# Kernel optimization log

Hardware: AMD Instinct MI355X
Metric: run time of the kernel (lower is better)

The kernel has to match this reference:

```python
import jax, jax.numpy as jnp
import numpy as np

V, E, H, D = 32000, 512, 512, 3          # vocab, embed_dim, hidden_dim, max_depth
PD = max(H // 4, 16)                      # policy depth-embed dim = 128
DEPTH_EMBED_SCALE = 0.01
SIB_SCALE = 1.0 / np.sqrt(H)              # sibling_scale default 1/sqrt(hidden_dim)
GREEDY_THRESHOLD = 0.5
PROB_MIN, PROB_MAX = 1e-7, 1.0 - 1e-7


def _ln(x, g, b, eps=1e-5):
    m = x.mean(-1, keepdims=True)
    v = jnp.var(x, axis=-1, keepdims=True)
    return (x - m) * jax.lax.rsqrt(v + eps) * g + b


def setup_inputs() -> dict:
    key = jax.random.key(0)
    ks = jax.random.split(key, 12)
    def n(k, shape, s=0.02):
        return jax.random.normal(k, shape, jnp.float32) * s
    return {
        "token_ids": jax.random.randint(ks[0], (4096,), 0, V),
        "emb": n(ks[1], (V, E)),                      # embedding table
        "proj_w": n(ks[2], (H, E), 0.04), "proj_b": jnp.zeros(H, jnp.float32),
        "cf_w": n(ks[3], (2 * H, H), 0.04), "cf_b": jnp.zeros(2 * H, jnp.float32),
        "in_g": jnp.ones(H, jnp.float32), "in_b": jnp.zeros(H, jnp.float32),   # policy input LayerNorm
        "pde": n(ks[4], (D + 1, PD), 0.01),           # policy depth embedding
        "f1w": n(ks[5], (H // 2, H + PD), 0.04), "f1b": jnp.zeros(H // 2, jnp.float32),
        "n1g": jnp.ones(H // 2, jnp.float32), "n1b": jnp.zeros(H // 2, jnp.float32),
        "f2w": n(ks[6], (H // 4, H // 2), 0.06), "f2b": jnp.zeros(H // 4, jnp.float32),
        "n2g": jnp.ones(H // 4, jnp.float32), "n2b": jnp.zeros(H // 4, jnp.float32),
        "pow_w": n(ks[7], (1, H // 4), 0.01), "pow_b": jnp.zeros(1, jnp.float32),
        "sib": n(ks[8], (2, H)),                      # sibling embeddings (left/right)
        "dep": n(ks[9], (D + 1, H), 0.01),            # tree depth embeddings
        "out_w": n(ks[10], (V, H), 0.04), "out_b": jnp.zeros(V, jnp.float32),
    }


def _forward(token_ids, emb, proj_w, proj_b, cf_w, cf_b, in_g, in_b, pde,
             f1w, f1b, n1g, n1b, f2w, f2b, n2g, n2b, pow_w, pow_b,
             sib, dep, out_w, out_b):
    # h0: project token embeddings to hidden space. [N, H]
    h0 = emb[token_ids] @ proj_w.T + proj_b
    nodes = h0[None]                      # level-0 nodes: [1, N, H]
    agg_sum = h0                          # running sum over all tree nodes
    agg_cnt = jnp.float32(1.0)
    alive = jnp.float32(1.0)              # cumulative greedy-expand mask
    for level in range(D):
        # growth policy on the level-mean hidden (+ scaled depth embedding)
        lh = nodes.mean(0) + DEPTH_EMBED_SCALE * dep[level]          # [N, H]
        hn = _ln(lh, in_g, in_b)
        de = jnp.broadcast_to(pde[min(level, D)], (hn.shape[0], PD))
        x = jnp.concatenate([hn, de], axis=-1)
        x = jax.nn.relu(_ln(x @ f1w.T + f1b, n1g, n1b))
        x = jax.nn.relu(_ln(x @ f2w.T + f2b, n2g, n2b))
        p = jax.nn.sigmoid((x @ pow_w.T + pow_b)[..., 0])             # [N]
        p_mean = jnp.clip(p, PROB_MIN, PROB_MAX).mean()
        alive = alive * (p_mean >= GREEDY_THRESHOLD).astype(jnp.float32)
        # binary child expansion: child_fc then chunk into left/right + sibling embeds
        cf = jnp.einsum('mnh,kh->mnk', nodes, cf_w) + cf_b            # [M, N, 2H]
        left = cf[..., :H] + SIB_SCALE * sib[0]
        right = cf[..., H:] + SIB_SCALE * sib[1]
        nodes = jnp.concatenate([left, right], axis=0)                # [2M, N, H]
        agg_sum = agg_sum + alive * nodes.sum(0)
        agg_cnt = agg_cnt + alive * jnp.float32(nodes.shape[0])
    pooled = agg_sum / jnp.maximum(agg_cnt, 1e-8)                     # mean pooling
    return pooled @ out_w.T + out_b                                   # [N, V]


def reference(token_ids, emb, proj_w, proj_b, cf_w, cf_b, in_g, in_b, pde,
              f1w, f1b, n1g, n1b, f2w, f2b, n2g, n2b, pow_w, pow_b,
              sib, dep, out_w, out_b):
    return _forward(token_ids, emb, proj_w, proj_b, cf_w, cf_b, in_g, in_b, pde,
                    f1w, f1b, n1g, n1b, f2w, f2b, n2g, n2b, pow_w, pow_b,
                    sib, dep, out_w, out_b)
```

## Files before the change

### kernel.cpp

```cpp
#include <hip/hip_runtime.h>

typedef unsigned short u16;
using bf16x8 = __attribute__((ext_vector_type(8))) short;
using f32x4  = __attribute__((ext_vector_type(4))) float;

#define SIB_SCALE_F 0.04419417382415922f

__device__ __forceinline__ u16 f2b(float f) {
  unsigned u = __builtin_bit_cast(unsigned, f);
  return (u16)((u + 0x7FFFu + ((u >> 16) & 1u)) >> 16);
}

__device__ __forceinline__ float wred(float v) {
  #pragma unroll
  for (int m = 1; m < 64; m <<= 1) v += __shfl_xor(v, m);
  return v;
}

__device__ __forceinline__ void gload16(const void* g, void* l) {
  __builtin_amdgcn_global_load_lds(
      (const __attribute__((address_space(1))) unsigned int*)g,
      (__attribute__((address_space(3))) unsigned int*)l, 16, 0, 0);
}

__global__ __launch_bounds__(256, 2) void gemmT(
    const u16* __restrict__ A, const u16* __restrict__ B,
    const float* __restrict__ bias,
    float* __restrict__ C, int M, int N, int K, int MT)
{
  __shared__ u16 lds[32768];
  const int t = threadIdx.x, w = t >> 6, lane = t & 63;
  const int wm = w >> 1, wn = w & 1;
  const int r16 = lane & 15, ks = lane >> 4;
  const int bn = blockIdx.y * 128;
  const int mg = blockIdx.x;
  const int stag = blockIdx.y & (MT - 1);

  auto stageT = [&](const u16* __restrict__ G, int grow0, int ktile, int buf, int base) {
    const int k0 = ktile << 6;
    u16* dst = lds + base + (buf << 13);
    #pragma unroll
    for (int j = 0; j < 4; ++j) {
      const int r = j * 32 + w * 8 + (lane >> 3);
      const int s = (lane & 7) ^ (r & 7);
      gload16(G + (size_t)(grow0 + r) * K + k0 + s * 8,
              dst + j * 2048 + w * 512);
    }
  };

  float4 biasv[4];
  #pragma unroll
  for (int n = 0; n < 4; ++n)
    biasv[n] = *(const float4*)(bias + bn + wn * 64 + n * 16 + ks * 4);

  f32x4 acc[4][4], pacc[4][4];
  #pragma unroll
  for (int m = 0; m < 4; ++m)
    #pragma unroll
    for (int n = 0; n < 4; ++n) {
      f32x4 z = {0.f, 0.f, 0.f, 0.f};
      acc[m][n] = z; pacc[m][n] = z;
    }
  int bmPrev = 0;

  {
    const int bm0 = (mg * MT + (stag & (MT - 1))) * 128;
    stageT(A, bm0, 0, 0, 0);
    stageT(B, bn, 0, 0, 16384);
    stageT(B, bn, 1, 1, 16384);
    asm volatile("s_waitcnt vmcnt(4)" ::: "memory");
    __builtin_amdgcn_sched_barrier(0);
    __builtin_amdgcn_s_barrier();
  }

  for (int mt = 0; mt < MT; ++mt) {
    const int bm = (mg * MT + ((mt + stag) & (MT - 1))) * 128;
    const int bmNext = (mg * MT + ((mt + 1 + stag) & (MT - 1))) * 128;

    #pragma unroll
    for (int kt = 0; kt < 8; ++kt) {
      const u16* Ab = lds + ((kt & 1) << 13);
      const u16* Bb = lds + 16384 + ((kt & 1) << 13);
      bf16x8 bfr[4][2];

      #pragma unroll
      for (int p = 0; p < 4; ++p) {
        bf16x8 af[2];
        {
          const int row = wm * 64 + p * 16 + r16;
          af[0] = *(const bf16x8*)(Ab + row * 64 + ((ks ^ (row & 7)) << 3));
          af[1] = *(const bf16x8*)(Ab + row * 64 + (((4 + ks) ^ (row & 7)) << 3));
        }
        if (p == 0) {
          #pragma unroll
          for (int n = 0; n < 4; ++n) {
            const int row = wn * 64 + n * 16 + r16;
            bfr[n][0] = *(const bf16x8*)(Bb + row * 64 + ((ks ^ (row & 7)) << 3));
            bfr[n][1] = *(const bf16x8*)(Bb + row * 64 + (((4 + ks) ^ (row & 7)) << 3));
          }
          if (kt < 7)             stageT(A, bm,     kt + 1, (kt + 1) & 1, 0);
          else if (mt < MT - 1)   stageT(A, bmNext, 0,      0,            0);
        }
        if (p == 1 && kt == 0 && mt > 0) {
          #pragma unroll
          for (int m = 0; m < 4; ++m) {
            const int grow = bmPrev + wm * 64 + m * 16 + r16;
            float* Crow = C + (size_t)grow * N;
            #pragma unroll
            for (int n = 0; n < 4; ++n) {
              const int gcol = bn + wn * 64 + n * 16 + ks * 4;
              f32x4 o;
              o[0] = pacc[m][n][0] + biasv[n].x;
              o[1] = pacc[m][n][1] + biasv[n].y;
              o[2] = pacc[m][n][2] + biasv[n].z;
              o[3] = pacc[m][n][3] + biasv[n].w;
              __builtin_nontemporal_store(o, (f32x4*)(Crow + gcol));
            }
          }
        }
        if (p == 2) {
          if (kt < 6)             stageT(B, bn, kt + 2,       kt & 1, 16384);
          else if (mt < MT - 1)   stageT(B, bn, (kt + 2) & 7, kt & 1, 16384);
        }
        if (p == 3) {
          if (kt == 0) {
            if (mt > 0) { asm volatile("s_waitcnt vmcnt(20)" ::: "memory"); }
            else        { asm volatile("s_waitcnt vmcnt(4)"  ::: "memory"); }
          } else if (kt < 6) {
            asm volatile("s_waitcnt vmcnt(4)" ::: "memory");
          } else if (kt == 6) {
            if (mt < MT - 1) { asm volatile("s_waitcnt vmcnt(4)" ::: "memory"); }
            else             { asm volatile("s_waitcnt vmcnt(0)" ::: "memory"); }
          } else {
            if (mt < MT - 1) { asm volatile("s_waitcnt vmcnt(4)" ::: "memory"); }
          }
          __builtin_amdgcn_sched_barrier(0);
        }
        __builtin_amdgcn_s_barrier();
        asm volatile("s_waitcnt lgkmcnt(0)" ::: "memory");
        __builtin_amdgcn_sched_barrier(0);
        __builtin_amdgcn_s_setprio(1);
        #pragma unroll
        for (int n = 0; n < 4; ++n) {
          acc[p][n] = __builtin_amdgcn_mfma_f32_16x16x32_bf16(bfr[n][0], af[0], acc[p][n], 0, 0, 0);
          acc[p][n] = __builtin_amdgcn_mfma_f32_16x16x32_bf16(bfr[n][1], af[1], acc[p][n], 0, 0, 0);
        }
        __builtin_amdgcn_s_setprio(0);
        __builtin_amdgcn_s_barrier();
      }
    }

    bmPrev = bm;
    #pragma unroll
    for (int m = 0; m < 4; ++m)
      #pragma unroll
      for (int n = 0; n < 4; ++n) {
        pacc[m][n] = acc[m][n];
        f32x4 z = {0.f, 0.f, 0.f, 0.f};
        acc[m][n] = z;
      }
  }

  #pragma unroll
  for (int m = 0; m < 4; ++m) {
    const int grow = bmPrev + wm * 64 + m * 16 + r16;
    float* Crow = C + (size_t)grow * N;
    #pragma unroll
    for (int n = 0; n < 4; ++n) {
      const int gcol = bn + wn * 64 + n * 16 + ks * 4;
      f32x4 o;
      o[0] = pacc[m][n][0] + biasv[n].x;
      o[1] = pacc[m][n][1] + biasv[n].y;
      o[2] = pacc[m][n][2] + biasv[n].z;
      o[3] = pacc[m][n][3] + biasv[n].w;
      __builtin_nontemporal_store(o, (f32x4*)(Crow + gcol));
    }
  }
}

template <bool GATHER>
__global__ __launch_bounds__(256) void gemm64(
    const float* __restrict__ Afp, const int* __restrict__ tok,
    const u16* __restrict__ A, const u16* __restrict__ B,
    const float* __restrict__ bias, int blvl, float bscale,
    float* __restrict__ C, u16* __restrict__ Cb,
    int M, int N, int K)
{
  __shared__ u16 ldsA[64 * 32];
  __shared__ u16 ldsB[128 * 32];
  const int t = threadIdx.x, w = t >> 6, lane = t & 63;
  const int r16 = lane & 15, ks = lane >> 4;

  const int nb = gridDim.x * gridDim.y;
  const int lid = blockIdx.y * gridDim.x + blockIdx.x;
  const int chunk = nb >> 3;
  const int nlid = (lid & 7) * chunk + (lid >> 3);
  const int bm = (nlid % gridDim.x) * 64;
  const int bn = (nlid / gridDim.x) * 128;

  const int srow = t >> 2, sslot = t & 3;

  f32x4 acc[4][2];
  #pragma unroll
  for (int m = 0; m < 4; ++m)
    #pragma unroll
    for (int n = 0; n < 2; ++n) {
      f32x4 z = {0.f, 0.f, 0.f, 0.f};
      acc[m][n] = z;
    }

  for (int k0 = 0; k0 < K; k0 += 32) {
    if (k0) __syncthreads();
    {
      const int row = srow;
      const int sl = sslot ^ ((row >> 1) & 3);
      if constexpr (GATHER) {
        const float* src = Afp + (size_t)tok[bm + row] * 512 + k0 + sl * 8;
        const float4 a0 = *(const float4*)src;
        const float4 a1 = *(const float4*)(src + 4);
        bf16x8 v;
        v[0] = (short)f2b(a0.x); v[1] = (short)f2b(a0.y);
        v[2] = (short)f2b(a0.z); v[3] = (short)f2b(a0.w);
        v[4] = (short)f2b(a1.x); v[5] = (short)f2b(a1.y);
        v[6] = (short)f2b(a1.z); v[7] = (short)f2b(a1.w);
        *(bf16x8*)(ldsA + t * 8) = v;
      } else {
        gload16(A + (size_t)(bm + row) * K + k0 + sl * 8, ldsA + w * 512);
      }
    }
    #pragma unroll
    for (int i = 0; i < 2; ++i) {
      const int row = i * 64 + srow;
      const int sl = sslot ^ ((row >> 1) & 3);
      gload16(B + (size_t)(bn + row) * K + k0 + sl * 8,
              ldsB + i * 2048 + w * 512);
    }
    __syncthreads();

    bf16x8 af[4], bfr[2];
    #pragma unroll
    for (int m = 0; m < 4; ++m) {
      const int row = m * 16 + r16;
      af[m] = *(const bf16x8*)(ldsA + row * 32 + ((ks ^ ((row >> 1) & 3)) << 3));
    }
    #pragma unroll
    for (int n = 0; n < 2; ++n) {
      const int row = w * 32 + n * 16 + r16;
      bfr[n] = *(const bf16x8*)(ldsB + row * 32 + ((ks ^ ((row >> 1) & 3)) << 3));
    }
    #pragma unroll
    for (int m = 0; m < 4; ++m)
      #pragma unroll
      for (int n = 0; n < 2; ++n)
        acc[m][n] = __builtin_amdgcn_mfma_f32_16x16x32_bf16(bfr[n], af[m], acc[m][n], 0, 0, 0);
  }

  const float* be = bias + (size_t)(bm >> 12) * blvl;
  #pragma unroll
  for (int m = 0; m < 4; ++m) {
    const int grow = bm + m * 16 + r16;
    #pragma unroll
    for (int n = 0; n < 2; ++n) {
      const int gcol = bn + w * 32 + n * 16 + ks * 4;
      const float4 bv = *(const float4*)(be + gcol);
      float4 o;
      o.x = acc[m][n][0] + bv.x * bscale;
      o.y = acc[m][n][1] + bv.y * bscale;
      o.z = acc[m][n][2] + bv.z * bscale;
      o.w = acc[m][n][3] + bv.w * bscale;
      const size_t idx = (size_t)grow * N + gcol;
      *(float4*)(C + idx) = o;
      if (Cb) {
        ushort4 ob = { f2b(o.x), f2b(o.y), f2b(o.z), f2b(o.w) };
        *(ushort4*)(Cb + idx) = ob;
      }
    }
  }
}

__global__ __launch_bounds__(256) void gemm_pool(
    const u16* __restrict__ A, const u16* __restrict__ B,
    const float* __restrict__ bias, float bscale,
    const float* __restrict__ h0f, const float* __restrict__ S1f,
    const float* __restrict__ S2f, const float* __restrict__ psum,
    u16* __restrict__ P,
    int M, int N, int K)
{
  __shared__ u16 ldsA[128 * 32];
  __shared__ u16 ldsB[128 * 32];
  const int t = threadIdx.x;
  const int w = t >> 6;
  const int lane = t & 63;
  const int wr = w >> 1, wc = w & 1;

  const int nb = gridDim.x * gridDim.y;
  const int lid = blockIdx.y * gridDim.x + blockIdx.x;
  const int chunk = nb >> 3;
  const int nlid = (lid & 7) * chunk + (lid >> 3);
  const int bx = nlid % gridDim.x, by = nlid / gridDim.x;

  const int bm = bx * 128, bn = by * 128;
  const int r16 = lane & 15, ks = lane >> 4;
  const int srow = t >> 2, sslot = t & 3;

  f32x4 acc[4][4];
  #pragma unroll
  for (int m = 0; m < 4; ++m)
    #pragma unroll
    for (int n = 0; n < 4; ++n) {
      f32x4 z = {0.f, 0.f, 0.f, 0.f};
      acc[m][n] = z;
    }

  for (int k0 = 0; k0 < K; k0 += 32) {
    if (k0) __syncthreads();
    #pragma unroll
    for (int i = 0; i < 2; ++i) {
      const int row = srow + i * 64;
      const int sl = sslot ^ ((row >> 1) & 3);
      gload16(A + (size_t)(bm + row) * K + k0 + sl * 8,
              ldsA + (i * 2048 + w * 512));
      gload16(B + (size_t)(bn + row) * K + k0 + sl * 8,
              ldsB + (i * 2048 + w * 512));
    }
    __syncthreads();

    bf16x8 af[4], bfr[4];
    #pragma unroll
    for (int m = 0; m < 4; ++m) {
      const int row = wr * 64 + m * 16 + r16;
      af[m] = *(const bf16x8*)(ldsA + row * 32 + ((ks ^ ((row >> 1) & 3)) << 3));
    }
    #pragma unroll
    for (int n = 0; n < 4; ++n) {
      const int row = wc * 64 + n * 16 + r16;
      bfr[n] = *(const bf16x8*)(ldsB + row * 32 + ((ks ^ ((row >> 1) & 3)) << 3));
    }
    #pragma unroll
    for (int m = 0; m < 4; ++m)
      #pragma unroll
      for (int n = 0; n < 4; ++n)
        acc[m][n] = __builtin_amdgcn_mfma_f32_16x16x32_bf16(bfr[n], af[m], acc[m][n], 0, 0, 0);
  }

  const float a0 = (psum[0] * (1.f / 4096.f) >= 0.5f) ? 1.f : 0.f;
  const float a1 = a0 * ((psum[1] * (1.f / 4096.f) >= 0.5f) ? 1.f : 0.f);
  const float a2 = a1 * ((psum[2] * (1.f / 4096.f) >= 0.5f) ? 1.f : 0.f);
  const float cnt = 1.f + a0 * 2.f + a1 * 4.f + a2 * 8.f;
  const float inv = 1.f / fmaxf(cnt, 1e-8f);

  #pragma unroll
  for (int m = 0; m < 4; ++m) {
    const int grow = bm + wr * 64 + m * 16 + r16;
    #pragma unroll
    for (int n = 0; n < 4; ++n) {
      const int gcol = bn + wc * 64 + n * 16 + ks * 4;
      const float4 bv = *(const float4*)(bias + gcol);
      float4 o;
      o.x = acc[m][n][0] + bv.x * bscale;
      o.y = acc[m][n][1] + bv.y * bscale;
      o.z = acc[m][n][2] + bv.z * bscale;
      o.w = acc[m][n][3] + bv.w * bscale;
      const size_t idx = (size_t)grow * N + gcol;
      const float4 h = *(const float4*)(h0f + idx);
      const float4 s1 = *(const float4*)(S1f + idx);
      const float4 s2 = *(const float4*)(S2f + idx);
      ushort4 ob;
      ob.x = f2b((h.x + a0 * s1.x + a1 * s2.x + a2 * o.x) * inv);
      ob.y = f2b((h.y + a0 * s1.y + a1 * s2.y + a2 * o.y) * inv);
      ob.z = f2b((h.z + a0 * s1.z + a1 * s2.z + a2 * o.z) * inv);
      ob.w = f2b((h.w + a0 * s1.w + a1 * s2.w + a2 * o.w) * inv);
      *(ushort4*)(P + idx) = ob;
    }
  }
}

__global__ __launch_bounds__(256) void prep_misc(
    const float* __restrict__ cf_w, const float* __restrict__ cf_b,
    const float* __restrict__ sib, const float* __restrict__ proj_w,
    const float* __restrict__ f1w, const float* __restrict__ f1b,
    const float* __restrict__ f2w, const float* __restrict__ pde,
    const float* __restrict__ out_w,
    u16* __restrict__ wsum_b, u16* __restrict__ projw_b,
    u16* __restrict__ f1w512b, u16* __restrict__ f2wb,
    float* __restrict__ cvec, float* __restrict__ psum,
    float* __restrict__ y1bias, u16* __restrict__ outw_b)
{
  const int b = blockIdx.x, t = threadIdx.x;
  if (b >= 676) {
    const int idx = (b - 676) * 256 + t;
    const float4 v = ((const float4*)out_w)[idx];
    ushort4 o = { f2b(v.x), f2b(v.y), f2b(v.z), f2b(v.w) };
    ((ushort4*)outw_b)[idx] = o;
  } else if (b < 256) {
    const int idx = b * 256 + t;
    const float4 a = ((const float4*)cf_w)[idx];
    const float4 c = ((const float4*)(cf_w + 262144))[idx];
    ushort4 o = { f2b(a.x + c.x), f2b(a.y + c.y), f2b(a.z + c.z), f2b(a.w + c.w) };
    ((ushort4*)wsum_b)[idx] = o;
  } else if (b < 512) {
    const int idx = (b - 256) * 256 + t;
    const float4 v = ((const float4*)proj_w)[idx];
    ushort4 o = { f2b(v.x), f2b(v.y), f2b(v.z), f2b(v.w) };
    ((ushort4*)projw_b)[idx] = o;
  } else if (b < 640) {
    const int fi = (b - 512) * 256 + t;
    const int row = fi >> 7, c4 = fi & 127;
    const float4 v = *(const float4*)(f1w + (size_t)row * 640 + c4 * 4);
    ushort4 o = { f2b(v.x), f2b(v.y), f2b(v.z), f2b(v.w) };
    ((ushort4*)f1w512b)[row * 128 + c4] = o;
  } else if (b < 672) {
    const int idx = (b - 640) * 256 + t;
    const float4 v = ((const float4*)f2w)[idx];
    ushort4 o = { f2b(v.x), f2b(v.y), f2b(v.z), f2b(v.w) };
    ((ushort4*)f2wb)[idx] = o;
  } else if (b < 675) {
    const int l = b - 672, j = t;
    const float* wrow = f1w + (size_t)j * 640 + 512;
    const float* p = pde + l * 128;
    float s = f1b[j];
    #pragma unroll 4
    for (int k = 0; k < 128; ++k) s += wrow[k] * p[k];
    y1bias[l * 256 + j] = s;
  } else {
    cvec[t]       = cf_b[t]       + cf_b[512 + t] + SIB_SCALE_F * (sib[t]       + sib[512 + t]);
    cvec[256 + t] = cf_b[256 + t] + cf_b[768 + t] + SIB_SCALE_F * (sib[256 + t] + sib[768 + t]);
    if (t < 3) psum[t] = 0.f;
  }
}

__global__ __launch_bounds__(256) void mean_ln_concat_b(
    const float* __restrict__ S0, const float* __restrict__ S1,
    const float* __restrict__ S2,
    const float* __restrict__ dep,
    const float* __restrict__ g, const float* __restrict__ b,
    u16* __restrict__ X)
{
  const int wid = threadIdx.x >> 6, lane = threadIdx.x & 63;
  const int gr = blockIdx.x * 4 + wid;
  const int l = gr >> 12, n = gr & 4095;
  const float* Sr = (l == 0 ? S0 : l == 1 ? S1 : S2) + (size_t)n * 512;
  const float invM = (l == 0 ? 1.f : l == 1 ? 0.5f : 0.25f);
  const float* depl = dep + 512 * l;
  const int c0 = lane * 8;
  float x[8];
  float s = 0.f, sq = 0.f;
  #pragma unroll
  for (int i = 0; i < 8; ++i) {
    const float v = Sr[c0 + i] * invM + 0.01f * depl[c0 + i];
    x[i] = v; s += v; sq += v * v;
  }
  s = wred(s); sq = wred(sq);
  const float mean = s * (1.f / 512.f);
  const float var = sq * (1.f / 512.f) - mean * mean;
  const float rs = rsqrtf(var + 1e-5f);
  ushort4 o0, o1;
  o0.x = f2b((x[0] - mean) * rs * g[c0 + 0] + b[c0 + 0]);
  o0.y = f2b((x[1] - mean) * rs * g[c0 + 1] + b[c0 + 1]);
  o0.z = f2b((x[2] - mean) * rs * g[c0 + 2] + b[c0 + 2]);
  o0.w = f2b((x[3] - mean) * rs * g[c0 + 3] + b[c0 + 3]);
  o1.x = f2b((x[4] - mean) * rs * g[c0 + 4] + b[c0 + 4]);
  o1.y = f2b((x[5] - mean) * rs * g[c0 + 5] + b[c0 + 5]);
  o1.z = f2b((x[6] - mean) * rs * g[c0 + 6] + b[c0 + 6]);
  o1.w = f2b((x[7] - mean) * rs * g[c0 + 7] + b[c0 + 7]);
  ushort4* Xr = (ushort4*)(X + (size_t)gr * 512);
  Xr[lane * 2]     = o0;
  Xr[lane * 2 + 1] = o1;
}

__global__ __launch_bounds__(256) void ln_relu_b256(
    const float* __restrict__ X, const float* __restrict__ g,
    const float* __restrict__ b, u16* __restrict__ O)
{
  const int wid = threadIdx.x >> 6, lane = threadIdx.x & 63;
  const int n = blockIdx.x * 4 + wid;
  const float* Xr = X + (size_t)n * 256;
  float x[4];
  float s = 0.f, sq = 0.f;
  #pragma unroll
  for (int i = 0; i < 4; ++i) {
    x[i] = Xr[lane * 4 + i]; s += x[i]; sq += x[i] * x[i];
  }
  s = wred(s); sq = wred(sq);
  const float mean = s * (1.f / 256.f);
  const float var = sq * (1.f / 256.f) - mean * mean;
  const float rs = rsqrtf(var + 1e-5f);
  ushort4 o;
  o.x = f2b(fmaxf((x[0] - mean) * rs * g[lane * 4 + 0] + b[lane * 4 + 0], 0.f));
  o.y = f2b(fmaxf((x[1] - mean) * rs * g[lane * 4 + 1] + b[lane * 4 + 1], 0.f));
  o.z = f2b(fmaxf((x[2] - mean) * rs * g[lane * 4 + 2] + b[lane * 4 + 2], 0.f));
  o.w = f2b(fmaxf((x[3] - mean) * rs * g[lane * 4 + 3] + b[lane * 4 + 3], 0.f));
  ((ushort4*)(O + (size_t)n * 256))[lane] = o;
}

__global__ __launch_bounds__(256) void ln_policy128(
    const float* __restrict__ Y2, const float* __restrict__ g,
    const float* __restrict__ b, const float* __restrict__ pw,
    const float* __restrict__ pb, float* __restrict__ psum)
{
  __shared__ float part[4];
  const int wid = threadIdx.x >> 6, lane = threadIdx.x & 63;
  const int gr = blockIdx.x * 4 + wid;
  const float* Xr = Y2 + (size_t)gr * 128;
  float x[2];
  float s = 0.f, sq = 0.f;
  #pragma unroll
  for (int i = 0; i < 2; ++i) {
    x[i] = Xr[lane * 2 + i]; s += x[i]; sq += x[i] * x[i];
  }
  s = wred(s); sq = wred(sq);
  const float mean = s * (1.f / 128.f);
  const float var = sq * (1.f / 128.f) - mean * mean;
  const float rs = rsqrtf(var + 1e-5f);
  float z = 0.f;
  #pragma unroll
  for (int i = 0; i < 2; ++i) {
    const int c = lane * 2 + i;
    const float v = fmaxf((x[i] - mean) * rs * g[c] + b[c], 0.f);
    z += v * pw[c];
  }
  z = wred(z);
  if (lane == 0) {
    const float p = 1.f / (1.f + expf(-(z + pb[0])));
    part[wid] = fminf(fmaxf(p, 1e-7f), 1.f - 1e-7f);
  }
  __syncthreads();
  if (threadIdx.x == 0)
    atomicAdd(psum + (gr >> 12), part[0] + part[1] + part[2] + part[3]);
}

extern "C" void kernel_launch(void* const* d_in, const int* in_sizes, int n_in,
                              void* d_out, int out_size, void* d_ws, size_t ws_size,
                              hipStream_t stream) {
  const int*   tok    = (const int*)  d_in[0];
  const float* emb    = (const float*)d_in[1];
  const float* proj_w = (const float*)d_in[2];
  const float* proj_b = (const float*)d_in[3];
  const float* cf_w   = (const float*)d_in[4];
  const float* cf_b   = (const float*)d_in[5];
  const float* in_g   = (const float*)d_in[6];
  const float* in_b   = (const float*)d_in[7];
  const float* pde    = (const float*)d_in[8];
  const float* f1w    = (const float*)d_in[9];
  const float* f1b    = (const float*)d_in[10];
  const float* n1g    = (const float*)d_in[11];
  const float* n1b    = (const float*)d_in[12];
  const float* f2w    = (const float*)d_in[13];
  const float* f2bias = (const float*)d_in[14];
  const float* n2g    = (const float*)d_in[15];
  const float* n2b    = (const float*)d_in[16];
  const float* pow_w  = (const float*)d_in[17];
  const float* pow_b  = (const float*)d_in[18];
  const float* sib    = (const float*)d_in[19];
  const float* dep    = (const float*)d_in[20];
  const float* out_w  = (const float*)d_in[21];
  const float* out_b  = (const float*)d_in[22];
  float* out = (float*)d_out;

  char* ws = (char*)d_ws;
  size_t off = 0;
  auto alloc = [&](size_t bytes) -> void* {
    void* p = ws + off;
    off += (bytes + 255) & ~(size_t)255;
    return p;
  };
  u16*   outw_b  = (u16*)  alloc((size_t)32000 * 512 * 2);
  u16*   projw_b = (u16*)  alloc((size_t)512 * 512 * 2);
  u16*   wsum_b  = (u16*)  alloc((size_t)512 * 512 * 2);
  u16*   f1w512b = (u16*)  alloc((size_t)256 * 512 * 2);
  u16*   f2wb    = (u16*)  alloc((size_t)128 * 256 * 2);
  float* h0f     = (float*)alloc((size_t)4096 * 512 * 4);
  u16*   h0b     = (u16*)  alloc((size_t)4096 * 512 * 2);
  float* S1f     = (float*)alloc((size_t)4096 * 512 * 4);
  u16*   S1b     = (u16*)  alloc((size_t)4096 * 512 * 2);
  float* S2f     = (float*)alloc((size_t)4096 * 512 * 4);
  u16*   S2b     = (u16*)  alloc((size_t)4096 * 512 * 2);
  u16*   X       = (u16*)  alloc((size_t)12288 * 512 * 2);
  float* Y1      = (float*)alloc((size_t)12288 * 256 * 4);
  u16*   Y1b     = (u16*)  alloc((size_t)12288 * 256 * 2);
  float* Y2      = (float*)alloc((size_t)12288 * 128 * 4);
  float* y1bias  = (float*)alloc(3 * 256 * 4);
  float* cvec    = (float*)alloc(512 * 4);
  float* psum    = (float*)alloc(256);
  u16*   poolb   = (u16*)  alloc((size_t)4096 * 512 * 2);

  prep_misc<<<16676, 256, 0, stream>>>(cf_w, cf_b, sib, proj_w, f1w, f1b, f2w,
                                       pde, out_w,
                                       wsum_b, projw_b, f1w512b, f2wb,
                                       cvec, psum, y1bias, outw_b);

  gemm64<true><<<dim3(64, 4), 256, 0, stream>>>(
      emb, tok, nullptr, projw_b, proj_b, 0, 1.f, h0f, h0b, 4096, 512, 512);
  gemm64<false><<<dim3(64, 4), 256, 0, stream>>>(
      nullptr, nullptr, h0b, wsum_b, cvec, 0, 1.f, S1f, S1b, 4096, 512, 512);
  gemm64<false><<<dim3(64, 4), 256, 0, stream>>>(
      nullptr, nullptr, S1b, wsum_b, cvec, 0, 2.f, S2f, S2b, 4096, 512, 512);

  mean_ln_concat_b<<<3072, 256, 0, stream>>>(h0f, S1f, S2f, dep, in_g, in_b, X);
  gemm64<false><<<dim3(192, 2), 256, 0, stream>>>(
      nullptr, nullptr, X, f1w512b, y1bias, 256, 1.f, Y1, nullptr, 12288, 256, 512);
  ln_relu_b256<<<3072, 256, 0, stream>>>(Y1, n1g, n1b, Y1b);
  gemm64<false><<<dim3(192, 1), 256, 0, stream>>>(
      nullptr, nullptr, Y1b, f2wb, f2bias, 0, 1.f, Y2, nullptr, 12288, 128, 256);
  ln_policy128<<<3072, 256, 0, stream>>>(Y2, n2g, n2b, pow_w, pow_b, psum);

  gemm_pool<<<dim3(32, 4), 256, 0, stream>>>(
      S2b, wsum_b, cvec, 4.f, h0f, S1f, S2f, psum, poolb, 4096, 512, 512);

  gemmT<<<dim3(2, 250), 256, 0, stream>>>(poolb, outw_b, out_b,
                                          out, 4096, 32000, 512, 16);
}
```

Measured before the change: 467.8 us.

## Keep full output-weight tile resident in LDS and stream activations through all M tiles

```diff
diff --git a/kernel.cpp b/kernel.cpp
--- a/kernel.cpp
+++ b/kernel.cpp
@@ -23,27 +23,32 @@
       (__attribute__((address_space(3))) unsigned int*)l, 16, 0, 0);
 }
 
-__global__ __launch_bounds__(256, 2) void gemmT(
+__global__ __launch_bounds__(256, 1) void gemmV(
     const u16* __restrict__ A, const u16* __restrict__ B,
     const float* __restrict__ bias,
-    float* __restrict__ C, int M, int N, int K, int MT)
+    float* __restrict__ C, int M, int N, int K)
 {
-  __shared__ u16 lds[32768];
+  __shared__ u16 lds[77824];
   const int t = threadIdx.x, w = t >> 6, lane = t & 63;
   const int wm = w >> 1, wn = w & 1;
   const int r16 = lane & 15, ks = lane >> 4;
-  const int bn = blockIdx.y * 128;
-  const int mg = blockIdx.x;
-  const int stag = blockIdx.y & (MT - 1);
-
-  auto stageT = [&](const u16* __restrict__ G, int grow0, int ktile, int buf, int base) {
-    const int k0 = ktile << 6;
-    u16* dst = lds + base + (buf << 13);
-    #pragma unroll
-    for (int j = 0; j < 4; ++j) {
-      const int r = j * 32 + w * 8 + (lane >> 3);
-      const int s = (lane & 7) ^ (r & 7);
-      gload16(G + (size_t)(grow0 + r) * K + k0 + s * 8,
+  const int bn = blockIdx.x * 128;
+  const int stag = blockIdx.x & 31;
+
+  #pragma unroll 4
+  for (int i = 0; i < 32; ++i) {
+    const int c = i * 4 + w;
+    const int ksrc = (lane & ~7) | ((lane & 7) ^ (c & 7));
+    gload16(B + (size_t)(bn + c) * 512 + ksrc * 8, lds + c * 512);
+  }
+
+  auto stageA = [&](int bmT, int kt, int buf) {
+    u16* dst = lds + 65536 + buf * 4096;
+    #pragma unroll
+    for (int j = 0; j < 2; ++j) {
+      const int r = j * 64 + w * 16 + (lane >> 2);
+      const int s = (lane & 3) ^ (r & 3);
+      gload16(A + (size_t)(bmT + r) * 512 + kt * 32 + s * 8,
               dst + j * 2048 + w * 512);
     }
   };
@@ -64,101 +69,91 @@
   int bmPrev = 0;
 
   {
-    const int bm0 = (mg * MT + (stag & (MT - 1))) * 128;
-    stageT(A, bm0, 0, 0, 0);
-    stageT(B, bn, 0, 0, 16384);
-    stageT(B, bn, 1, 1, 16384);
-    asm volatile("s_waitcnt vmcnt(4)" ::: "memory");
+    const int bm0 = (stag & 31) * 128;
+    stageA(bm0, 0, 0);
+    stageA(bm0, 1, 1);
+    asm volatile("s_waitcnt vmcnt(2)" ::: "memory");
     __builtin_amdgcn_sched_barrier(0);
-    __builtin_amdgcn_s_barrier();
-  }
-
-  for (int mt = 0; mt < MT; ++mt) {
-    const int bm = (mg * MT + ((mt + stag) & (MT - 1))) * 128;
-    const int bmNext = (mg * MT + ((mt + 1 + stag) & (MT - 1))) * 128;
-
-    #pragma unroll
-    for (int kt = 0; kt < 8; ++kt) {
-      const u16* Ab = lds + ((kt & 1) << 13);
-      const u16* Bb = lds + 16384 + ((kt & 1) << 13);
-      bf16x8 bfr[4][2];
-
+  }
+
+  int bufR = 0;
+  for (int mt = 0; mt < 32; ++mt) {
+    const int bm  = ((mt + stag) & 31) * 128;
+    const int bmN = ((mt + 1 + stag) & 31) * 128;
+
+    #pragma unroll
+    for (int kt = 0; kt < 16; ++kt) {
+      const int g = mt * 16 + kt;
+      if (g > 0) {
+        if (g == 511) asm volatile("s_waitcnt vmcnt(0)" ::: "memory");
+        else          asm volatile("s_waitcnt vmcnt(2)" ::: "memory");
+        __builtin_amdgcn_sched_barrier(0);
+      }
+      __builtin_amdgcn_s_barrier();
+
+      const u16* Ab = lds + 65536 + bufR * 4096;
+      bf16x8 af[4], bfr[4];
       #pragma unroll
-      for (int p = 0; p < 4; ++p) {
-        bf16x8 af[2];
-        {
-          const int row = wm * 64 + p * 16 + r16;
-          af[0] = *(const bf16x8*)(Ab + row * 64 + ((ks ^ (row & 7)) << 3));
-          af[1] = *(const bf16x8*)(Ab + row * 64 + (((4 + ks) ^ (row & 7)) << 3));
-        }
-        if (p == 0) {
+      for (int m = 0; m < 4; ++m) {
+        const int row = wm * 64 + m * 16 + r16;
+        af[m] = *(const bf16x8*)(Ab + row * 32 + ((ks ^ (row & 3)) << 3));
+      }
+      #pragma unroll
+      for (int n = 0; n < 4; ++n) {
+        const int col = wn * 64 + n * 16 + r16;
+        bfr[n] = *(const bf16x8*)(lds + col * 512 + (kt >> 1) * 64 +
+                                  ((((kt & 1) * 4 + ks) ^ (col & 7)) << 3));
+      }
+
+      if (kt == 0 && mt > 0) {
+        __builtin_amdgcn_sched_barrier(0);
+        #pragma unroll
+        for (int m = 0; m < 4; ++m) {
+          const int grow = bmPrev + wm * 64 + m * 16 + r16;
+          float* Crow = C + (size_t)grow * N;
           #pragma unroll
           for (int n = 0; n < 4; ++n) {
-            const int row = wn * 64 + n * 16 + r16;
-            bfr[n][0] = *(const bf16x8*)(Bb + row * 64 + ((ks ^ (row & 7)) << 3));
-            bfr[n][1] = *(const bf16x8*)(Bb + row * 64 + (((4 + ks) ^ (row & 7)) << 3));
-          }
-          if (kt < 7)             stageT(A, bm,     kt + 1, (kt + 1) & 1, 0);
-          else if (mt < MT - 1)   stageT(A, bmNext, 0,      0,            0);
-        }
-        if (p == 1 && kt == 0 && mt > 0) {
-          #pragma unroll
-          for (int m = 0; m < 4; ++m) {
-            const int grow = bmPrev + wm * 64 + m * 16 + r16;
-            float* Crow = C + (size_t)grow * N;
-            #pragma unroll
-            for (int n = 0; n < 4; ++n) {
-              const int gcol = bn + wn * 64 + n * 16 + ks * 4;
-              f32x4 o;
-              o[0] = pacc[m][n][0] + biasv[n].x;
-              o[1] = pacc[m][n][1] + biasv[n].y;
-              o[2] = pacc[m][n][2] + biasv[n].z;
-              o[3] = pacc[m][n][3] + biasv[n].w;
-              __builtin_nontemporal_store(o, (f32x4*)(Crow + gcol));
-            }
+            const int gcol = bn + wn * 64 + n * 16 + ks * 4;
+            float4 o;
+            o.x = pacc[m][n][0] + biasv[n].x;
+            o.y = pacc[m][n][1] + biasv[n].y;
+            o.z = pacc[m][n][2] + biasv[n].z;
+            o.w = pacc[m][n][3] + biasv[n].w;
+            *(float4*)(Crow + gcol) = o;
           }
         }
-        if (p == 2) {
-          if (kt < 6)             stageT(B, bn, kt + 2,       kt & 1, 16384);
-          else if (mt < MT - 1)   stageT(B, bn, (kt + 2) & 7, kt & 1, 16384);
-        }
-        if (p == 3) {
-          if (kt == 0) {
-            if (mt > 0) { asm volatile("s_waitcnt vmcnt(20)" ::: "memory"); }
-            else        { asm volatile("s_waitcnt vmcnt(4)"  ::: "memory"); }
-          } else if (kt < 6) {
-            asm volatile("s_waitcnt vmcnt(4)" ::: "memory");
-          } else if (kt == 6) {
-            if (mt < MT - 1) { asm volatile("s_waitcnt vmcnt(4)" ::: "memory"); }
-            else             { asm volatile("s_waitcnt vmcnt(0)" ::: "memory"); }
-          } else {
-            if (mt < MT - 1) { asm volatile("s_waitcnt vmcnt(4)" ::: "memory"); }
+        __builtin_amdgcn_sched_barrier(0);
+      }
+
+      if (g + 2 < 512) {
+        const int kt2 = kt + 2;
+        const int bm2 = (kt2 < 16) ? bm : bmN;
+        stageA(bm2, kt2 & 15, (bufR + 2) % 3);
+      }
+
+      asm volatile("s_waitcnt lgkmcnt(0)" ::: "memory");
+      __builtin_amdgcn_sched_barrier(0);
+      __builtin_amdgcn_s_setprio(1);
+      #pragma unroll
+      for (int m = 0; m < 4; ++m)
+        #pragma unroll
+        for (int n = 0; n < 4; ++n)
+          acc[m][n] = __builtin_amdgcn_mfma_f32_16x16x32_bf16(bfr[n], af[m], acc[m][n], 0, 0, 0);
+      __builtin_amdgcn_s_setprio(0);
+
+      if (kt == 15) {
+        bmPrev = bm;
+        #pragma unroll
+        for (int m = 0; m < 4; ++m)
+          #pragma unroll
+          for (int n = 0; n < 4; ++n) {
+            pacc[m][n] = acc[m][n];
+            f32x4 z = {0.f, 0.f, 0.f, 0.f};
+            acc[m][n] = z;
           }
-          __builtin_amdgcn_sched_barrier(0);
-        }
-        __builtin_amdgcn_s_barrier();
-        asm volatile("s_waitcnt lgkmcnt(0)" ::: "memory");
-        __builtin_amdgcn_sched_barrier(0);
-        __builtin_amdgcn_s_setprio(1);
-        #pragma unroll
-        for (int n = 0; n < 4; ++n) {
-          acc[p][n] = __builtin_amdgcn_mfma_f32_16x16x32_bf16(bfr[n][0], af[0], acc[p][n], 0, 0, 0);
-          acc[p][n] = __builtin_amdgcn_mfma_f32_16x16x32_bf16(bfr[n][1], af[1], acc[p][n], 0, 0, 0);
-        }
-        __builtin_amdgcn_s_setprio(0);
-        __builtin_amdgcn_s_barrier();
-      }
-    }
-
-    bmPrev = bm;
-    #pragma unroll
-    for (int m = 0; m < 4; ++m)
-      #pragma unroll
-      for (int n = 0; n < 4; ++n) {
-        pacc[m][n] = acc[m][n];
-        f32x4 z = {0.f, 0.f, 0.f, 0.f};
-        acc[m][n] = z;
-      }
+      }
+      bufR = (bufR + 1) % 3;
+    }
   }
 
   #pragma unroll
@@ -168,12 +163,12 @@
     #pragma unroll
     for (int n = 0; n < 4; ++n) {
       const int gcol = bn + wn * 64 + n * 16 + ks * 4;
-      f32x4 o;
-      o[0] = pacc[m][n][0] + biasv[n].x;
-      o[1] = pacc[m][n][1] + biasv[n].y;
-      o[2] = pacc[m][n][2] + biasv[n].z;
-      o[3] = pacc[m][n][3] + biasv[n].w;
-      __builtin_nontemporal_store(o, (f32x4*)(Crow + gcol));
+      float4 o;
+      o.x = pacc[m][n][0] + biasv[n].x;
+      o.y = pacc[m][n][1] + biasv[n].y;
+      o.z = pacc[m][n][2] + biasv[n].z;
+      o.w = pacc[m][n][3] + biasv[n].w;
+      *(float4*)(Crow + gcol) = o;
     }
   }
 }
@@ -607,6 +602,5 @@
   gemm_pool<<<dim3(32, 4), 256, 0, stream>>>(
       S2b, wsum_b, cvec, 4.f, h0f, S1f, S2f, psum, poolb, 4096, 512, 512);
 
-  gemmT<<<dim3(2, 250), 256, 0, stream>>>(poolb, outw_b, out_b,
-                                          out, 4096, 32000, 512, 16);
-}
+  gemmV<<<250, 256, 0, stream>>>(poolb, outw_b, out_b, out, 4096, 32000, 512);
+}
```

Measured after the change: 397.6 us. 15.0% less time.
